# Performance work log

Measured on AMD Instinct MI355X. Metric: run time of the kernel, lower is better.

Reference implementation:

```python
import jax, jax.numpy as jnp
import numpy as np

D_MODEL = 512
D_VALUE = 512
N_HEADS = 8
NEG_INF = -1e30


def _layernorm(x, g, b, eps=1e-5):
    mu = jnp.mean(x, axis=-1, keepdims=True)
    var = jnp.var(x, axis=-1, keepdims=True)
    return (x - mu) * jax.lax.rsqrt(var + eps) * g + b


def setup_inputs() -> dict:
    key = jax.random.key(0)
    ks = jax.random.split(key, 16)
    B, L, dq = 4, 2048, 512
    d_model, d_value, H = D_MODEL, D_VALUE, N_HEADS
    d4 = 4 * d_model
    s = lambda d: 1.0 / np.sqrt(d)
    inp = {
        "q": jax.random.normal(ks[0], (B, L, dq), jnp.float32),
        "k": jax.random.normal(ks[1], (B, L, dq), jnp.float32),
        "v": jax.random.normal(ks[2], (B, L, d_value), jnp.float32),
        "Wq": jax.random.normal(ks[3], (d_model, dq), jnp.float32) * s(dq),
        "bq": jnp.zeros((d_model,), jnp.float32),
        "Wk": jax.random.normal(ks[4], (d_model, dq), jnp.float32) * s(dq),
        "bk": jnp.zeros((d_model,), jnp.float32),
        "Wv": jax.random.normal(ks[5], (d_model, d_value), jnp.float32) * s(d_value),
        "bv": jnp.zeros((d_model,), jnp.float32),
        "Wo": jax.random.normal(ks[6], (d_value, d_model), jnp.float32) * s(d_model),
        "bo": jnp.zeros((d_value,), jnp.float32),
        "Wc1": jax.random.normal(ks[7], (d4, d_value), jnp.float32) * s(d_value),
        "bc1": jnp.zeros((d4,), jnp.float32),
        "Wc2": jax.random.normal(ks[8], (d_value, d4), jnp.float32) * s(d4),
        "bc2": jnp.zeros((d_value,), jnp.float32),
        "g1": jnp.ones((d_value,), jnp.float32),
        "b1": jnp.zeros((d_value,), jnp.float32),
        "g2": jnp.ones((d_value,), jnp.float32),
        "b2": jnp.zeros((d_value,), jnp.float32),
        "Wl": jax.random.normal(ks[9], (d_model, d_value), jnp.float32) * s(d_value),
        "bl": jnp.zeros((d_model,), jnp.float32),
    }
    return inp


def reference(q, k, v, Wq, bq, Wk, bk, Wv, bv, Wo, bo, Wc1, bc1, Wc2, bc2,
              g1, b1, g2, b2, Wl, bl):
    B, L, _ = q.shape
    S = k.shape[1]
    H = N_HEADS
    E = D_MODEL // H
    # projections -> [B, L, H, E]
    queries = (q @ Wq.T + bq).reshape(B, L, H, E)
    keys = (k @ Wk.T + bk).reshape(B, S, H, E)
    values = (v @ Wv.T + bv).reshape(B, S, H, E)
    # naive causal attention, full [B,H,L,S] scores
    scale = 1.0 / np.sqrt(E)
    scores = jnp.einsum('blhe,bshe->bhls', queries, keys)
    causal = jnp.triu(jnp.ones((L, S), dtype=bool), k=1)  # True above diagonal
    scores = jnp.where(causal, NEG_INF, scores)
    A = jax.nn.softmax(scale * scores, axis=-1)
    att = jnp.einsum('bhls,bshd->blhd', A, values).reshape(B, L, H * E)
    att = att @ Wo.T + bo
    # residual + FFN (conv1d kernel_size=1 == pointwise linear)
    x = _layernorm(v + att, g1, b1)
    y = jax.nn.relu(x @ Wc1.T + bc1)
    y = y @ Wc2.T + bc2
    y = _layernorm(x + y, g2, b2)
    return y @ Wl.T + bl
```

## Files before the change

kernel.cpp:

```cpp
#include <hip/hip_runtime.h>
#include <hip/hip_bf16.h>


typedef __attribute__((ext_vector_type(8))) short sh8;
typedef __attribute__((ext_vector_type(4))) float f32x4;

#define QSCALE 0.18033688011110543f

__device__ __forceinline__ void storeOut(float* p, float v) { *p = v; }
__device__ __forceinline__ void storeOut(__hip_bfloat16* p, float v) { *p = __float2bfloat16(v); }

__device__ __forceinline__ void gl_lds16(const void* g, void* l) {
    __builtin_amdgcn_global_load_lds((const __attribute__((address_space(1))) void*)g,
                                     (__attribute__((address_space(3))) void*)l, 16, 0, 0);
}

__device__ __forceinline__ unsigned pk_bf16(float a, float b) {
    __hip_bfloat162 h = __float22bfloat162_rn(make_float2(a, b));
    return *(unsigned*)&h;
}
__device__ __forceinline__ sh8 pk8(float4 a, float4 b) {
    int4 iv = make_int4(pk_bf16(a.x, a.y), pk_bf16(a.z, a.w),
                        pk_bf16(b.x, b.y), pk_bf16(b.z, b.w));
    return *(sh8*)&iv;
}

struct WArg { const float* w[7]; unsigned short* wd; };
__global__ __launch_bounds__(256) void conv_w(WArg p)
{
    const int i = (blockIdx.x * 256 + threadIdx.x) * 4;
    if (i >= 3407872) return;
    const float* s; int off;
    if      (i < 262144)  { s = p.w[0]; off = i; }
    else if (i < 524288)  { s = p.w[1]; off = i - 262144; }
    else if (i < 786432)  { s = p.w[2]; off = i - 524288; }
    else if (i < 1048576) { s = p.w[3]; off = i - 786432; }
    else if (i < 1310720) { s = p.w[4]; off = i - 1048576; }
    else if (i < 2359296) { s = p.w[5]; off = i - 1310720; }
    else                  { s = p.w[6]; off = i - 2359296; }
    const float4 v = *(const float4*)(s + off);
    *(uint2*)(p.wd + i) = make_uint2(pk_bf16(v.x, v.y), pk_bf16(v.z, v.w));
}

struct QkvArg {
    const float *A0, *A1, *A2;
    const float *b0, *b1, *b2;
    unsigned short *C0, *C1;
    unsigned short *Vt;
};
__global__ __launch_bounds__(256) void gemm_qkv(QkvArg ar, const unsigned short* __restrict__ Wall,
                                                int M, int N, int K)
{
    const int z = blockIdx.z;
    const float* A = z == 0 ? ar.A0 : (z == 1 ? ar.A1 : ar.A2);
    const unsigned short* W = Wall + (size_t)z * 262144;
    const float* bias = z == 0 ? ar.b0 : (z == 1 ? ar.b1 : ar.b2);

    __shared__ float AsF[8192];
    __shared__ unsigned short BsL[8192];
    const int t    = threadIdx.x;
    const int wave = t >> 6, lane = t & 63;
    const int quad = lane >> 4, col = lane & 15;
    const int wm   = wave >> 1, wn = wave & 1;
    const int m0   = blockIdx.y * 128, n0 = blockIdx.x * 128;

    f32x4 acc[4][4];
    #pragma unroll
    for (int mt = 0; mt < 4; mt++)
        #pragma unroll
        for (int nt = 0; nt < 4; nt++)
            acc[mt][nt] = (f32x4){0.f, 0.f, 0.f, 0.f};

    for (int k0 = 0; k0 < K; k0 += 64) {
        #pragma unroll
        for (int seg = 0; seg < 8; seg++) {
            const int r0  = (seg * 4 + wave) * 4;
            const int row = r0 + (lane >> 4);
            const int ck  = (lane & 15) ^ (row & 15);
            gl_lds16(A + (size_t)(m0 + row) * K + k0 + ck * 4, &AsF[r0 * 64]);
        }
        #pragma unroll
        for (int seg = 0; seg < 4; seg++) {
            const int r0  = (seg * 4 + wave) * 8;
            const int row = r0 + (lane >> 3);
            const int ck  = (lane & 7) ^ (row & 7);
            gl_lds16(W + (size_t)(n0 + row) * K + k0 + ck * 8, &BsL[r0 * 64]);
        }
        __syncthreads();
        #pragma unroll
        for (int kc = 0; kc < 2; kc++) {
            sh8 af[4], bf[4];
            #pragma unroll
            for (int mt = 0; mt < 4; mt++) {
                const int mr  = wm * 64 + mt * 16 + col;
                const int q0  = kc * 8 + quad * 2;
                const int m16 = mr & 15;
                float4 f0 = *(const float4*)&AsF[mr * 64 + ((q0 ^ m16) << 2)];
                float4 f1 = *(const float4*)&AsF[mr * 64 + (((q0 + 1) ^ m16) << 2)];
                af[mt] = pk8(f0, f1);
            }
            #pragma unroll
            for (int nt = 0; nt < 4; nt++) {
                const int nr = wn * 64 + nt * 16 + col;
                bf[nt] = *(const sh8*)&BsL[nr * 64 + (((kc * 4 + quad) ^ (nr & 7)) << 3)];
            }
            #pragma unroll
            for (int mt = 0; mt < 4; mt++)
                #pragma unroll
                for (int nt = 0; nt < 4; nt++)
                    acc[mt][nt] = __builtin_amdgcn_mfma_f32_16x16x32_bf16(af[mt], bf[nt], acc[mt][nt], 0, 0, 0);
        }
        __syncthreads();
    }

    if (z < 2) {
        unsigned short* C = z == 0 ? ar.C0 : ar.C1;
        const float scale = z == 0 ? QSCALE : 1.0f;
        #pragma unroll
        for (int nt = 0; nt < 4; nt++) {
            const int cn = n0 + wn * 64 + nt * 16 + col;
            const float bj = bias[cn];
            #pragma unroll
            for (int mt = 0; mt < 4; mt++) {
                const int rm = m0 + wm * 64 + mt * 16 + quad * 4;
                #pragma unroll
                for (int reg = 0; reg < 4; reg++)
                    C[(size_t)(rm + reg) * N + cn] =
                        (unsigned short)__bfloat16_as_ushort(__float2bfloat16((acc[mt][nt][reg] + bj) * scale));
            }
        }
    } else {
        const int b = m0 >> 11;
        #pragma unroll
        for (int nt = 0; nt < 4; nt++) {
            const int cn = n0 + wn * 64 + nt * 16 + col;
            const int h = cn >> 6, e = cn & 63;
            const float bj = bias[cn];
            #pragma unroll
            for (int mt = 0; mt < 4; mt++) {
                const int s0r = (m0 + wm * 64 + mt * 16 + quad * 4) & 2047;
                float cv[4];
                #pragma unroll
                for (int reg = 0; reg < 4; reg++) cv[reg] = acc[mt][nt][reg] + bj;
                *(uint2*)(ar.Vt + ((size_t)(b * 8 + h) * 64 + e) * 2048 + s0r) =
                    make_uint2(pk_bf16(cv[0], cv[1]), pk_bf16(cv[2], cv[3]));
            }
        }
    }
}

template <typename TOUT, bool RELU>
__global__ __launch_bounds__(256) void gemm_mfma(const unsigned short* __restrict__ A,
                                                 const unsigned short* __restrict__ W,
                                                 const float* __restrict__ bias,
                                                 TOUT* __restrict__ C,
                                                 int M, int N, int K)
{
    __shared__ unsigned short AsL[8192];
    __shared__ unsigned short BsL[8192];
    const int t    = threadIdx.x;
    const int wave = t >> 6, lane = t & 63;
    const int quad = lane >> 4, col = lane & 15;
    const int wm   = wave >> 1, wn = wave & 1;
    const int m0   = blockIdx.y * 128, n0 = blockIdx.x * 128;

    f32x4 acc[4][4];
    #pragma unroll
    for (int mt = 0; mt < 4; mt++)
        #pragma unroll
        for (int nt = 0; nt < 4; nt++)
            acc[mt][nt] = (f32x4){0.f, 0.f, 0.f, 0.f};

    for (int k0 = 0; k0 < K; k0 += 64) {
        #pragma unroll
        for (int seg = 0; seg < 4; seg++) {
            const int r0  = (seg * 4 + wave) * 8;
            const int row = r0 + (lane >> 3);
            const int ck  = (lane & 7) ^ (row & 7);
            gl_lds16(A + (size_t)(m0 + row) * K + k0 + ck * 8, &AsL[r0 * 64]);
            gl_lds16(W + (size_t)(n0 + row) * K + k0 + ck * 8, &BsL[r0 * 64]);
        }
        __syncthreads();
        #pragma unroll
        for (int kc = 0; kc < 2; kc++) {
            sh8 af[4], bf[4];
            #pragma unroll
            for (int mt = 0; mt < 4; mt++) {
                const int ar = wm * 64 + mt * 16 + col;
                af[mt] = *(const sh8*)&AsL[ar * 64 + (((kc * 4 + quad) ^ (ar & 7)) << 3)];
            }
            #pragma unroll
            for (int nt = 0; nt < 4; nt++) {
                const int nr = wn * 64 + nt * 16 + col;
                bf[nt] = *(const sh8*)&BsL[nr * 64 + (((kc * 4 + quad) ^ (nr & 7)) << 3)];
            }
            #pragma unroll
            for (int mt = 0; mt < 4; mt++)
                #pragma unroll
                for (int nt = 0; nt < 4; nt++)
                    acc[mt][nt] = __builtin_amdgcn_mfma_f32_16x16x32_bf16(af[mt], bf[nt], acc[mt][nt], 0, 0, 0);
        }
        __syncthreads();
    }
    #pragma unroll
    for (int nt = 0; nt < 4; nt++) {
        const int cn = n0 + wn * 64 + nt * 16 + col;
        const float bj = bias[cn];
        #pragma unroll
        for (int mt = 0; mt < 4; mt++) {
            const int rm = m0 + wm * 64 + mt * 16 + quad * 4;
            #pragma unroll
            for (int reg = 0; reg < 4; reg++) {
                float cv = acc[mt][nt][reg] + bj;
                if (RELU) cv = fmaxf(cv, 0.f);
                storeOut(&C[(size_t)(rm + reg) * N + cn], cv);
            }
        }
    }
}

template <typename TOUT, bool RELU>
__global__ __launch_bounds__(256) void gemm_mfma64(const unsigned short* __restrict__ A,
                                                   const unsigned short* __restrict__ W,
                                                   const float* __restrict__ bias,
                                                   TOUT* __restrict__ C,
                                                   int M, int N, int K)
{
    __shared__ unsigned short AsL[4096];
    __shared__ unsigned short BsL[8192];
    const int t    = threadIdx.x;
    const int wave = t >> 6, lane = t & 63;
    const int quad = lane >> 4, col = lane & 15;
    const int wm   = wave >> 1, wn = wave & 1;
    const int m0   = blockIdx.y * 64, n0 = blockIdx.x * 128;

    f32x4 acc[2][4];
    #pragma unroll
    for (int mt = 0; mt < 2; mt++)
        #pragma unroll
        for (int nt = 0; nt < 4; nt++)
            acc[mt][nt] = (f32x4){0.f, 0.f, 0.f, 0.f};

    for (int k0 = 0; k0 < K; k0 += 64) {
        #pragma unroll
        for (int seg = 0; seg < 2; seg++) {
            const int r0  = (seg * 4 + wave) * 8;
            const int row = r0 + (lane >> 3);
            const int ck  = (lane & 7) ^ (row & 7);
            gl_lds16(A + (size_t)(m0 + row) * K + k0 + ck * 8, &AsL[r0 * 64]);
        }
        #pragma unroll
        for (int seg = 0; seg < 4; seg++) {
            const int r0  = (seg * 4 + wave) * 8;
            const int row = r0 + (lane >> 3);
            const int ck  = (lane & 7) ^ (row & 7);
            gl_lds16(W + (size_t)(n0 + row) * K + k0 + ck * 8, &BsL[r0 * 64]);
        }
        __syncthreads();
        #pragma unroll
        for (int kc = 0; kc < 2; kc++) {
            sh8 af[2], bf[4];
            #pragma unroll
            for (int mt = 0; mt < 2; mt++) {
                const int ar = wm * 32 + mt * 16 + col;
                af[mt] = *(const sh8*)&AsL[ar * 64 + (((kc * 4 + quad) ^ (ar & 7)) << 3)];
            }
            #pragma unroll
            for (int nt = 0; nt < 4; nt++) {
                const int nr = wn * 64 + nt * 16 + col;
                bf[nt] = *(const sh8*)&BsL[nr * 64 + (((kc * 4 + quad) ^ (nr & 7)) << 3)];
            }
            #pragma unroll
            for (int mt = 0; mt < 2; mt++)
                #pragma unroll
                for (int nt = 0; nt < 4; nt++)
                    acc[mt][nt] = __builtin_amdgcn_mfma_f32_16x16x32_bf16(af[mt], bf[nt], acc[mt][nt], 0, 0, 0);
        }
        __syncthreads();
    }
    #pragma unroll
    for (int nt = 0; nt < 4; nt++) {
        const int cn = n0 + wn * 64 + nt * 16 + col;
        const float bj = bias[cn];
        #pragma unroll
        for (int mt = 0; mt < 2; mt++) {
            const int rm = m0 + wm * 32 + mt * 16 + quad * 4;
            #pragma unroll
            for (int reg = 0; reg < 4; reg++) {
                float cv = acc[mt][nt][reg] + bj;
                if (RELU) cv = fmaxf(cv, 0.f);
                storeOut(&C[(size_t)(rm + reg) * N + cn], cv);
            }
        }
    }
}

__global__ __launch_bounds__(256, 2) void attn_mfma(const unsigned short* __restrict__ Qb,
                                                    const unsigned short* __restrict__ Kb,
                                                    const unsigned short* __restrict__ Vt,
                                                    __hip_bfloat16* __restrict__ O,
                                                    int L)
{
    __shared__ unsigned short Ks[2][4096];
    __shared__ unsigned short Vs[2][4096];
    __shared__ unsigned short PsA[4][16][72];
    __shared__ unsigned short PsB[4][16][72];

    const int i    = blockIdx.x;
    const int bh   = blockIdx.y;
    const int b    = bh >> 3, h = bh & 7;
    const int t    = threadIdx.x;
    const int w    = t >> 6, lane = t & 63;
    const int quad = lane >> 4, col = lane & 15;

    const int qtA = i, qtB = 31 - i;
    const int qrowA = qtA * 64 + w * 16 + col;
    const int qrowB = qtB * 64 + w * 16 + col;
    const int S = 32 - i;

    const int srow = lane >> 3;
    const int scp  = lane & 7;

    sh8 qfA[2], qfB[2];
    {
        const size_t qa = ((size_t)(b * L + qrowA) * 8 + h) * 64;
        qfA[0] = *(const sh8*)(Qb + qa + quad * 8);
        qfA[1] = *(const sh8*)(Qb + qa + 32 + quad * 8);
        const size_t qb2 = ((size_t)(b * L + qrowB) * 8 + h) * 64;
        qfB[0] = *(const sh8*)(Qb + qb2 + quad * 8);
        qfB[1] = *(const sh8*)(Qb + qb2 + 32 + quad * 8);
    }

    f32x4 OA[4], OB[4];
    #pragma unroll
    for (int nt = 0; nt < 4; nt++) { OA[nt] = (f32x4){0.f,0.f,0.f,0.f}; OB[nt] = (f32x4){0.f,0.f,0.f,0.f}; }
    float lA = 0.f, lB = 0.f;

    {
        #pragma unroll
        for (int seg = 0; seg < 2; seg++) {
            const int r0  = (seg * 4 + w) * 8;
            const int row = r0 + srow;
            const int ck  = scp ^ (row & 7);
            gl_lds16(Kb + ((size_t)(b * L + row) * 8 + h) * 64 + ck * 8, &Ks[0][r0 * 64]);
            gl_lds16(Vt + (size_t)(bh * 64 + row) * L + ck * 8, &Vs[0][r0 * 64]);
        }
        __syncthreads();
    }

    int cur = 0;
    for (int r = 0; r < S; r++) {
        if (r + 1 < S) {
            const int k1 = (r + 1) * 64;
            #pragma unroll
            for (int seg = 0; seg < 2; seg++) {
                const int r0  = (seg * 4 + w) * 8;
                const int row = r0 + srow;
                const int ck  = scp ^ (row & 7);
                gl_lds16(Kb + ((size_t)(b * L + k1 + row) * 8 + h) * 64 + ck * 8, &Ks[cur ^ 1][r0 * 64]);
                gl_lds16(Vt + (size_t)(bh * 64 + row) * L + k1 + ck * 8, &Vs[cur ^ 1][r0 * 64]);
            }
        }

        const int k0 = r * 64;
        const bool actA  = (r <= i);
        const bool maskA = (r == i);
        const bool maskB = (r == S - 1);

        f32x4 stA[4], stB[4];
        const f32x4 zz = {0.f, 0.f, 0.f, 0.f};
        #pragma unroll
        for (int ntk = 0; ntk < 4; ntk++) {
            const int key = ntk * 16 + col;
            const int sw  = key & 7;
            sh8 kf0 = *(const sh8*)&Ks[cur][key * 64 + ((quad ^ sw) << 3)];
            sh8 kf1 = *(const sh8*)&Ks[cur][key * 64 + (((quad + 4) ^ sw) << 3)];
            f32x4 aB = __builtin_amdgcn_mfma_f32_16x16x32_bf16(kf0, qfB[0], zz, 0, 0, 0);
            stB[ntk] = __builtin_amdgcn_mfma_f32_16x16x32_bf16(kf1, qfB[1], aB, 0, 0, 0);
            if (actA) {
                f32x4 aA = __builtin_amdgcn_mfma_f32_16x16x32_bf16(kf0, qfA[0], zz, 0, 0, 0);
                stA[ntk] = __builtin_amdgcn_mfma_f32_16x16x32_bf16(kf1, qfA[1], aA, 0, 0, 0);
            }
        }

        {
            if (maskB) {
                #pragma unroll
                for (int ntk = 0; ntk < 4; ntk++)
                    #pragma unroll
                    for (int reg = 0; reg < 4; reg++)
                        if (k0 + ntk * 16 + quad * 4 + reg > qrowB) stB[ntk][reg] = -1e30f;
            }
            #pragma unroll
            for (int ntk = 0; ntk < 4; ntk++) {
                #pragma unroll
                for (int reg = 0; reg < 4; reg++)
                    stB[ntk][reg] = exp2f(stB[ntk][reg]);
                lB += (stB[ntk][0] + stB[ntk][1]) + (stB[ntk][2] + stB[ntk][3]);
                *(uint2*)&PsB[w][col][ntk * 16 + quad * 4] =
                    make_uint2(pk_bf16(stB[ntk][0], stB[ntk][1]), pk_bf16(stB[ntk][2], stB[ntk][3]));
            }
        }
        if (actA) {
            if (maskA) {
                #pragma unroll
                for (int ntk = 0; ntk < 4; ntk++)
                    #pragma unroll
                    for (int reg = 0; reg < 4; reg++)
                        if (k0 + ntk * 16 + quad * 4 + reg > qrowA) stA[ntk][reg] = -1e30f;
            }
            #pragma unroll
            for (int ntk = 0; ntk < 4; ntk++) {
                #pragma unroll
                for (int reg = 0; reg < 4; reg++)
                    stA[ntk][reg] = exp2f(stA[ntk][reg]);
                lA += (stA[ntk][0] + stA[ntk][1]) + (stA[ntk][2] + stA[ntk][3]);
                *(uint2*)&PsA[w][col][ntk * 16 + quad * 4] =
                    make_uint2(pk_bf16(stA[ntk][0], stA[ntk][1]), pk_bf16(stA[ntk][2], stA[ntk][3]));
            }
        }

        #pragma unroll
        for (int kchunk = 0; kchunk < 2; kchunk++) {
            sh8 pfB = *(const sh8*)&PsB[w][col][kchunk * 32 + quad * 8];
            sh8 pfA;
            if (actA) pfA = *(const sh8*)&PsA[w][col][kchunk * 32 + quad * 8];
            #pragma unroll
            for (int nt = 0; nt < 4; nt++) {
                const int e  = nt * 16 + col;
                sh8 vf = *(const sh8*)&Vs[cur][e * 64 + (((kchunk * 4 + quad) ^ (e & 7)) << 3)];
                OB[nt] = __builtin_amdgcn_mfma_f32_16x16x32_bf16(pfB, vf, OB[nt], 0, 0, 0);
                if (actA) OA[nt] = __builtin_amdgcn_mfma_f32_16x16x32_bf16(pfA, vf, OA[nt], 0, 0, 0);
            }
        }
        __syncthreads();
        cur ^= 1;
    }

    lA += __shfl_xor(lA, 16); lA += __shfl_xor(lA, 32);
    lB += __shfl_xor(lB, 16); lB += __shfl_xor(lB, 32);
    {
        const float li = 1.f / lA;
        float lr[4];
        #pragma unroll
        for (int reg = 0; reg < 4; reg++) lr[reg] = __shfl(li, quad * 4 + reg);
        #pragma unroll
        for (int reg = 0; reg < 4; reg++) {
            const int qr = qtA * 64 + w * 16 + quad * 4 + reg;
            #pragma unroll
            for (int nt = 0; nt < 4; nt++)
                O[((size_t)(b * L + qr) * 8 + h) * 64 + nt * 16 + col] =
                    __float2bfloat16(OA[nt][reg] * lr[reg]);
        }
    }
    {
        const float li = 1.f / lB;
        float lr[4];
        #pragma unroll
        for (int reg = 0; reg < 4; reg++) lr[reg] = __shfl(li, quad * 4 + reg);
        #pragma unroll
        for (int reg = 0; reg < 4; reg++) {
            const int qr = qtB * 64 + w * 16 + quad * 4 + reg;
            #pragma unroll
            for (int nt = 0; nt < 4; nt++)
                O[((size_t)(b * L + qr) * 8 + h) * 64 + nt * 16 + col] =
                    __float2bfloat16(OB[nt][reg] * lr[reg]);
        }
    }
}

__global__ __launch_bounds__(256) void layernorm_k(const float* __restrict__ f1,
                                                   const float* __restrict__ f2,
                                                   const float* __restrict__ rb,
                                                   const float* __restrict__ g,
                                                   const float* __restrict__ bb,
                                                   float* __restrict__ out32,
                                                   __hip_bfloat16* __restrict__ out16)
{
    const int row = blockIdx.x;
    const int t   = threadIdx.x;
    const size_t base = (size_t)row * 512;
    const int i0 = t * 2;

    float a0 = f1[base + i0], a1 = f1[base + i0 + 1];
    if (f2) { a0 += f2[base + i0]; a1 += f2[base + i0 + 1]; }
    if (rb) { a0 += rb[base + i0]; a1 += rb[base + i0 + 1]; }

    float s = a0 + a1, ss = a0 * a0 + a1 * a1;
    #pragma unroll
    for (int off = 32; off > 0; off >>= 1) {
        s  += __shfl_xor(s, off);
        ss += __shfl_xor(ss, off);
    }
    __shared__ float red[16];
    const int lane = t & 63, wid = t >> 6;
    if (lane == 0) { red[wid] = s; red[8 + wid] = ss; }
    __syncthreads();
    if (t == 0) {
        const float S  = red[0] + red[1] + red[2] + red[3];
        const float SS = red[8] + red[9] + red[10] + red[11];
        const float mu = S * (1.f / 512.f);
        const float var = SS * (1.f / 512.f) - mu * mu;
        red[0] = mu;
        red[1] = rsqrtf(fmaxf(var, 0.f) + 1e-5f);
    }
    __syncthreads();
    const float mu = red[0], rstd = red[1];
    const float y0 = (a0 - mu) * rstd * g[i0]     + bb[i0];
    const float y1 = (a1 - mu) * rstd * g[i0 + 1] + bb[i0 + 1];
    if (out32) { out32[base + i0] = y0; out32[base + i0 + 1] = y1; }
    if (out16) { out16[base + i0] = __float2bfloat16(y0); out16[base + i0 + 1] = __float2bfloat16(y1); }
}

extern "C" void kernel_launch(void* const* d_in, const int* in_sizes, int n_in,
                              void* d_out, int out_size, void* d_ws, size_t ws_size,
                              hipStream_t stream)
{
    const float* q   = (const float*)d_in[0];
    const float* k   = (const float*)d_in[1];
    const float* v   = (const float*)d_in[2];
    const float* Wq  = (const float*)d_in[3];
    const float* bq  = (const float*)d_in[4];
    const float* Wk  = (const float*)d_in[5];
    const float* bk  = (const float*)d_in[6];
    const float* Wv  = (const float*)d_in[7];
    const float* bv  = (const float*)d_in[8];
    const float* Wo  = (const float*)d_in[9];
    const float* bo  = (const float*)d_in[10];
    const float* Wc1 = (const float*)d_in[11];
    const float* bc1 = (const float*)d_in[12];
    const float* Wc2 = (const float*)d_in[13];
    const float* bc2 = (const float*)d_in[14];
    const float* g1  = (const float*)d_in[15];
    const float* b1  = (const float*)d_in[16];
    const float* g2  = (const float*)d_in[17];
    const float* b2  = (const float*)d_in[18];
    const float* Wl  = (const float*)d_in[19];
    const float* bl  = (const float*)d_in[20];
    float* out = (float*)d_out;

    const int B = 4, L = 2048, H = 8;
    const int M = B * L;

    char* base = (char*)d_ws;
    unsigned short* Wall = (unsigned short*)(base + 0);
    unsigned short* Wob  = (unsigned short*)(base + 1572864);
    unsigned short* Wlb  = (unsigned short*)(base + 2097152);
    unsigned short* Wc1b = (unsigned short*)(base + 2621440);
    unsigned short* Wc2b = (unsigned short*)(base + 4718592);
    unsigned short* Qb   = (unsigned short*)(base + 6815744);
    unsigned short* Kb   = (unsigned short*)(base + 15204352);
    unsigned short* Vt   = (unsigned short*)(base + 23592960);
    unsigned short* A1   = (unsigned short*)(base + 31981568);
    float*          A2   = (float*)(base + 40370176);
    float*          X1   = (float*)(base + 57147392);
    unsigned short* X1b  = (unsigned short*)(base + 73924608);
    unsigned short* X2b  = (unsigned short*)(base + 73924608);
    unsigned short* H1   = (unsigned short*)(base + 6815744);
    float*          Y2   = (float*)(base + 40370176);

    const dim3 blk(256);

    WArg wa;
    wa.w[0] = Wq; wa.w[1] = Wk; wa.w[2] = Wv; wa.w[3] = Wo; wa.w[4] = Wl;
    wa.w[5] = Wc1; wa.w[6] = Wc2; wa.wd = Wall;
    conv_w<<<dim3(3328), blk, 0, stream>>>(wa);

    QkvArg qa;
    qa.A0 = q;  qa.A1 = k;  qa.A2 = v;
    qa.b0 = bq; qa.b1 = bk; qa.b2 = bv;
    qa.C0 = Qb; qa.C1 = Kb; qa.Vt = Vt;
    gemm_qkv<<<dim3(4, 64, 3), blk, 0, stream>>>(qa, Wall, M, 512, 512);

    attn_mfma<<<dim3(16, B * H), blk, 0, stream>>>(Qb, Kb, Vt, (__hip_bfloat16*)A1, L);

    gemm_mfma64<float, false><<<dim3(4, 128), blk, 0, stream>>>(A1, Wob, bo, A2, M, 512, 512);

    layernorm_k<<<dim3(M), blk, 0, stream>>>(A2, nullptr, v, g1, b1, X1, (__hip_bfloat16*)X1b);

    gemm_mfma<__hip_bfloat16, true><<<dim3(16, 64), blk, 0, stream>>>(X1b, Wc1b, bc1, (__hip_bfloat16*)H1, M, 2048, 512);

    gemm_mfma64<float, false><<<dim3(4, 128), blk, 0, stream>>>(H1, Wc2b, bc2, Y2, M, 512, 2048);

    layernorm_k<<<dim3(M), blk, 0, stream>>>(X1, Y2, nullptr, g2, b2, nullptr, (__hip_bfloat16*)X2b);

    gemm_mfma64<float, false><<<dim3(4, 128), blk, 0, stream>>>(X2b, Wlb, bl, out, M, 512, 512);
}
```

Measured before the change: 323.5 us.

## Load K/V fragments directly from global into registers, drop LDS staging

The attention kernel no longer stages K and V tiles in double-buffered LDS with async global-to-LDS loads and per-iteration barriers. Each wave now loads its own K and V MFMA fragments straight from global memory into registers and prefetches the next tile right after use. This removes the LDS traffic and __syncthreads. In exchange, all four waves redundantly fetch the same K/V data from global/L2, the reads are no longer swizzled or coalesced, and register pressure rises. It also hardcodes the strides 512 and 2048 in place of L.

```diff
diff --git a/kernel.cpp b/kernel.cpp
--- a/kernel.cpp
+++ b/kernel.cpp
@@ -301,8 +301,6 @@
                                                     __hip_bfloat16* __restrict__ O,
                                                     int L)
 {
-    __shared__ unsigned short Ks[2][4096];
-    __shared__ unsigned short Vs[2][4096];
     __shared__ unsigned short PsA[4][16][72];
     __shared__ unsigned short PsB[4][16][72];
 
@@ -317,9 +315,6 @@
     const int qrowA = qtA * 64 + w * 16 + col;
     const int qrowB = qtB * 64 + w * 16 + col;
     const int S = 32 - i;
-
-    const int srow = lane >> 3;
-    const int scp  = lane & 7;
 
     sh8 qfA[2], qfB[2];
     {
@@ -331,37 +326,29 @@
         qfB[1] = *(const sh8*)(Qb + qb2 + 32 + quad * 8);
     }
 
+    const unsigned short* kbase = Kb + ((size_t)(b * L + col)) * 512 + h * 64 + quad * 8;
+    const unsigned short* vbase = Vt + ((size_t)(bh * 64 + col)) * 2048 + quad * 8;
+
+    sh8 kf[8];
+    sh8 vf[8];
+
+    #pragma unroll
+    for (int ntk = 0; ntk < 4; ntk++) {
+        kf[ntk * 2]     = *(const sh8*)(kbase + (size_t)(ntk * 16) * 512);
+        kf[ntk * 2 + 1] = *(const sh8*)(kbase + (size_t)(ntk * 16) * 512 + 32);
+    }
+    #pragma unroll
+    for (int kc = 0; kc < 2; kc++)
+        #pragma unroll
+        for (int nt = 0; nt < 4; nt++)
+            vf[kc * 4 + nt] = *(const sh8*)(vbase + (size_t)(nt * 16) * 2048 + kc * 32);
+
     f32x4 OA[4], OB[4];
     #pragma unroll
     for (int nt = 0; nt < 4; nt++) { OA[nt] = (f32x4){0.f,0.f,0.f,0.f}; OB[nt] = (f32x4){0.f,0.f,0.f,0.f}; }
     float lA = 0.f, lB = 0.f;
 
-    {
-        #pragma unroll
-        for (int seg = 0; seg < 2; seg++) {
-            const int r0  = (seg * 4 + w) * 8;
-            const int row = r0 + srow;
-            const int ck  = scp ^ (row & 7);
-            gl_lds16(Kb + ((size_t)(b * L + row) * 8 + h) * 64 + ck * 8, &Ks[0][r0 * 64]);
-            gl_lds16(Vt + (size_t)(bh * 64 + row) * L + ck * 8, &Vs[0][r0 * 64]);
-        }
-        __syncthreads();
-    }
-
-    int cur = 0;
     for (int r = 0; r < S; r++) {
-        if (r + 1 < S) {
-            const int k1 = (r + 1) * 64;
-            #pragma unroll
-            for (int seg = 0; seg < 2; seg++) {
-                const int r0  = (seg * 4 + w) * 8;
-                const int row = r0 + srow;
-                const int ck  = scp ^ (row & 7);
-                gl_lds16(Kb + ((size_t)(b * L + k1 + row) * 8 + h) * 64 + ck * 8, &Ks[cur ^ 1][r0 * 64]);
-                gl_lds16(Vt + (size_t)(bh * 64 + row) * L + k1 + ck * 8, &Vs[cur ^ 1][r0 * 64]);
-            }
-        }
-
         const int k0 = r * 64;
         const bool actA  = (r <= i);
         const bool maskA = (r == i);
@@ -371,15 +358,20 @@
         const f32x4 zz = {0.f, 0.f, 0.f, 0.f};
         #pragma unroll
         for (int ntk = 0; ntk < 4; ntk++) {
-            const int key = ntk * 16 + col;
-            const int sw  = key & 7;
-            sh8 kf0 = *(const sh8*)&Ks[cur][key * 64 + ((quad ^ sw) << 3)];
-            sh8 kf1 = *(const sh8*)&Ks[cur][key * 64 + (((quad + 4) ^ sw) << 3)];
-            f32x4 aB = __builtin_amdgcn_mfma_f32_16x16x32_bf16(kf0, qfB[0], zz, 0, 0, 0);
-            stB[ntk] = __builtin_amdgcn_mfma_f32_16x16x32_bf16(kf1, qfB[1], aB, 0, 0, 0);
+            f32x4 aB = __builtin_amdgcn_mfma_f32_16x16x32_bf16(kf[ntk * 2], qfB[0], zz, 0, 0, 0);
+            stB[ntk] = __builtin_amdgcn_mfma_f32_16x16x32_bf16(kf[ntk * 2 + 1], qfB[1], aB, 0, 0, 0);
             if (actA) {
-                f32x4 aA = __builtin_amdgcn_mfma_f32_16x16x32_bf16(kf0, qfA[0], zz, 0, 0, 0);
-                stA[ntk] = __builtin_amdgcn_mfma_f32_16x16x32_bf16(kf1, qfA[1], aA, 0, 0, 0);
+                f32x4 aA = __builtin_amdgcn_mfma_f32_16x16x32_bf16(kf[ntk * 2], qfA[0], zz, 0, 0, 0);
+                stA[ntk] = __builtin_amdgcn_mfma_f32_16x16x32_bf16(kf[ntk * 2 + 1], qfA[1], aA, 0, 0, 0);
+            }
+        }
+
+        if (r + 1 < S) {
+            const unsigned short* kb2 = kbase + (size_t)(r + 1) * 64 * 512;
+            #pragma unroll
+            for (int ntk = 0; ntk < 4; ntk++) {
+                kf[ntk * 2]     = *(const sh8*)(kb2 + (size_t)(ntk * 16) * 512);
+                kf[ntk * 2 + 1] = *(const sh8*)(kb2 + (size_t)(ntk * 16) * 512 + 32);
             }
         }
 
@@ -427,14 +419,19 @@
             if (actA) pfA = *(const sh8*)&PsA[w][col][kchunk * 32 + quad * 8];
             #pragma unroll
             for (int nt = 0; nt < 4; nt++) {
-                const int e  = nt * 16 + col;
-                sh8 vf = *(const sh8*)&Vs[cur][e * 64 + (((kchunk * 4 + quad) ^ (e & 7)) << 3)];
-                OB[nt] = __builtin_amdgcn_mfma_f32_16x16x32_bf16(pfB, vf, OB[nt], 0, 0, 0);
-                if (actA) OA[nt] = __builtin_amdgcn_mfma_f32_16x16x32_bf16(pfA, vf, OA[nt], 0, 0, 0);
-            }
-        }
-        __syncthreads();
-        cur ^= 1;
+                OB[nt] = __builtin_amdgcn_mfma_f32_16x16x32_bf16(pfB, vf[kchunk * 4 + nt], OB[nt], 0, 0, 0);
+                if (actA) OA[nt] = __builtin_amdgcn_mfma_f32_16x16x32_bf16(pfA, vf[kchunk * 4 + nt], OA[nt], 0, 0, 0);
+            }
+        }
+
+        if (r + 1 < S) {
+            const unsigned short* vb2 = vbase + (r + 1) * 64;
+            #pragma unroll
+            for (int kc = 0; kc < 2; kc++)
+                #pragma unroll
+                for (int nt = 0; nt < 4; nt++)
+                    vf[kc * 4 + nt] = *(const sh8*)(vb2 + (size_t)(nt * 16) * 2048 + kc * 32);
+        }
     }
 
     lA += __shfl_xor(lA, 16); lA += __shfl_xor(lA, 32);
```

After: 386.4 us. +19.5%, slower.

## Split attention KV range across two blocks and add combine kernel

Applied to the files above, without the earlier changes.

Each attention block's key range is split into two halves handled by separate blocks (split-K), doubling grid size from 512 to 1024 blocks so more CUs are busy. Partial unnormalized outputs and row sums are written in fp32 to workspace, and a new combine kernel sums them, normalizes, and writes bf16. The change also drops K/V double-buffering in favor of a single buffer with a sync per tile, and shares one P scratch buffer between the two query tiles. It adds extra fp32 global traffic and a kernel launch, and may expose load latency now that prefetch is gone.

```diff
diff --git a/kernel.cpp b/kernel.cpp
--- a/kernel.cpp
+++ b/kernel.cpp
@@ -298,15 +298,17 @@
 __global__ __launch_bounds__(256, 2) void attn_mfma(const unsigned short* __restrict__ Qb,
                                                     const unsigned short* __restrict__ Kb,
                                                     const unsigned short* __restrict__ Vt,
-                                                    __hip_bfloat16* __restrict__ O,
+                                                    float* __restrict__ Op,
+                                                    float* __restrict__ Lp,
                                                     int L)
 {
-    __shared__ unsigned short Ks[2][4096];
-    __shared__ unsigned short Vs[2][4096];
-    __shared__ unsigned short PsA[4][16][72];
-    __shared__ unsigned short PsB[4][16][72];
-
-    const int i    = blockIdx.x;
+    __shared__ unsigned short Ks[4096];
+    __shared__ unsigned short Vs[4096];
+    __shared__ unsigned short Ps[4][16][72];
+
+    const int x    = blockIdx.x;
+    const int i    = x >> 1;
+    const int sp   = x & 1;
     const int bh   = blockIdx.y;
     const int b    = bh >> 3, h = bh & 7;
     const int t    = threadIdx.x;
@@ -316,7 +318,10 @@
     const int qtA = i, qtB = 31 - i;
     const int qrowA = qtA * 64 + w * 16 + col;
     const int qrowB = qtB * 64 + w * 16 + col;
-    const int S = 32 - i;
+    const int S  = 32 - i;
+    const int h0 = (S + 1) >> 1;
+    const int r0 = sp ? h0 : 0;
+    const int r1 = sp ? S : h0;
 
     const int srow = lane >> 3;
     const int scp  = lane & 7;
@@ -336,33 +341,18 @@
     for (int nt = 0; nt < 4; nt++) { OA[nt] = (f32x4){0.f,0.f,0.f,0.f}; OB[nt] = (f32x4){0.f,0.f,0.f,0.f}; }
     float lA = 0.f, lB = 0.f;
 
-    {
+    for (int r = r0; r < r1; r++) {
+        const int k0 = r * 64;
         #pragma unroll
         for (int seg = 0; seg < 2; seg++) {
-            const int r0  = (seg * 4 + w) * 8;
-            const int row = r0 + srow;
+            const int rr  = (seg * 4 + w) * 8;
+            const int row = rr + srow;
             const int ck  = scp ^ (row & 7);
-            gl_lds16(Kb + ((size_t)(b * L + row) * 8 + h) * 64 + ck * 8, &Ks[0][r0 * 64]);
-            gl_lds16(Vt + (size_t)(bh * 64 + row) * L + ck * 8, &Vs[0][r0 * 64]);
-        }
-        __syncthreads();
-    }
-
-    int cur = 0;
-    for (int r = 0; r < S; r++) {
-        if (r + 1 < S) {
-            const int k1 = (r + 1) * 64;
-            #pragma unroll
-            for (int seg = 0; seg < 2; seg++) {
-                const int r0  = (seg * 4 + w) * 8;
-                const int row = r0 + srow;
-                const int ck  = scp ^ (row & 7);
-                gl_lds16(Kb + ((size_t)(b * L + k1 + row) * 8 + h) * 64 + ck * 8, &Ks[cur ^ 1][r0 * 64]);
-                gl_lds16(Vt + (size_t)(bh * 64 + row) * L + k1 + ck * 8, &Vs[cur ^ 1][r0 * 64]);
-            }
-        }
-
-        const int k0 = r * 64;
+            gl_lds16(Kb + ((size_t)(b * L + k0 + row) * 8 + h) * 64 + ck * 8, &Ks[rr * 64]);
+            gl_lds16(Vt + (size_t)(bh * 64 + row) * L + k0 + ck * 8, &Vs[rr * 64]);
+        }
+        __syncthreads();
+
         const bool actA  = (r <= i);
         const bool maskA = (r == i);
         const bool maskB = (r == S - 1);
@@ -373,8 +363,8 @@
         for (int ntk = 0; ntk < 4; ntk++) {
             const int key = ntk * 16 + col;
             const int sw  = key & 7;
-            sh8 kf0 = *(const sh8*)&Ks[cur][key * 64 + ((quad ^ sw) << 3)];
-            sh8 kf1 = *(const sh8*)&Ks[cur][key * 64 + (((quad + 4) ^ sw) << 3)];
+            sh8 kf0 = *(const sh8*)&Ks[key * 64 + ((quad ^ sw) << 3)];
+            sh8 kf1 = *(const sh8*)&Ks[key * 64 + (((quad + 4) ^ sw) << 3)];
             f32x4 aB = __builtin_amdgcn_mfma_f32_16x16x32_bf16(kf0, qfB[0], zz, 0, 0, 0);
             stB[ntk] = __builtin_amdgcn_mfma_f32_16x16x32_bf16(kf1, qfB[1], aB, 0, 0, 0);
             if (actA) {
@@ -397,10 +387,21 @@
                 for (int reg = 0; reg < 4; reg++)
                     stB[ntk][reg] = exp2f(stB[ntk][reg]);
                 lB += (stB[ntk][0] + stB[ntk][1]) + (stB[ntk][2] + stB[ntk][3]);
-                *(uint2*)&PsB[w][col][ntk * 16 + quad * 4] =
+                *(uint2*)&Ps[w][col][ntk * 16 + quad * 4] =
                     make_uint2(pk_bf16(stB[ntk][0], stB[ntk][1]), pk_bf16(stB[ntk][2], stB[ntk][3]));
             }
-        }
+            #pragma unroll
+            for (int kchunk = 0; kchunk < 2; kchunk++) {
+                sh8 pf = *(const sh8*)&Ps[w][col][kchunk * 32 + quad * 8];
+                #pragma unroll
+                for (int nt = 0; nt < 4; nt++) {
+                    const int e = nt * 16 + col;
+                    sh8 vf = *(const sh8*)&Vs[e * 64 + (((kchunk * 4 + quad) ^ (e & 7)) << 3)];
+                    OB[nt] = __builtin_amdgcn_mfma_f32_16x16x32_bf16(pf, vf, OB[nt], 0, 0, 0);
+                }
+            }
+        }
+
         if (actA) {
             if (maskA) {
                 #pragma unroll
@@ -415,58 +416,60 @@
                 for (int reg = 0; reg < 4; reg++)
                     stA[ntk][reg] = exp2f(stA[ntk][reg]);
                 lA += (stA[ntk][0] + stA[ntk][1]) + (stA[ntk][2] + stA[ntk][3]);
-                *(uint2*)&PsA[w][col][ntk * 16 + quad * 4] =
+                *(uint2*)&Ps[w][col][ntk * 16 + quad * 4] =
                     make_uint2(pk_bf16(stA[ntk][0], stA[ntk][1]), pk_bf16(stA[ntk][2], stA[ntk][3]));
             }
-        }
-
-        #pragma unroll
-        for (int kchunk = 0; kchunk < 2; kchunk++) {
-            sh8 pfB = *(const sh8*)&PsB[w][col][kchunk * 32 + quad * 8];
-            sh8 pfA;
-            if (actA) pfA = *(const sh8*)&PsA[w][col][kchunk * 32 + quad * 8];
-            #pragma unroll
-            for (int nt = 0; nt < 4; nt++) {
-                const int e  = nt * 16 + col;
-                sh8 vf = *(const sh8*)&Vs[cur][e * 64 + (((kchunk * 4 + quad) ^ (e & 7)) << 3)];
-                OB[nt] = __builtin_amdgcn_mfma_f32_16x16x32_bf16(pfB, vf, OB[nt], 0, 0, 0);
-                if (actA) OA[nt] = __builtin_amdgcn_mfma_f32_16x16x32_bf16(pfA, vf, OA[nt], 0, 0, 0);
-            }
-        }
-        __syncthreads();
-        cur ^= 1;
+            #pragma unroll
+            for (int kchunk = 0; kchunk < 2; kchunk++) {
+                sh8 pf = *(const sh8*)&Ps[w][col][kchunk * 32 + quad * 8];
+                #pragma unroll
+                for (int nt = 0; nt < 4; nt++) {
+                    const int e = nt * 16 + col;
+                    sh8 vf = *(const sh8*)&Vs[e * 64 + (((kchunk * 4 + quad) ^ (e & 7)) << 3)];
+                    OA[nt] = __builtin_amdgcn_mfma_f32_16x16x32_bf16(pf, vf, OA[nt], 0, 0, 0);
+                }
+            }
+        }
+        __syncthreads();
     }
 
     lA += __shfl_xor(lA, 16); lA += __shfl_xor(lA, 32);
     lB += __shfl_xor(lB, 16); lB += __shfl_xor(lB, 32);
     {
-        const float li = 1.f / lA;
-        float lr[4];
-        #pragma unroll
-        for (int reg = 0; reg < 4; reg++) lr[reg] = __shfl(li, quad * 4 + reg);
+        float* Od = Op + (size_t)sp * 4194304;
+        float* Ld = Lp + (size_t)sp * 65536;
+        if (quad == 0) {
+            Ld[(size_t)(b * L + qtA * 64 + w * 16 + col) * 8 + h] = lA;
+            Ld[(size_t)(b * L + qtB * 64 + w * 16 + col) * 8 + h] = lB;
+        }
         #pragma unroll
         for (int reg = 0; reg < 4; reg++) {
-            const int qr = qtA * 64 + w * 16 + quad * 4 + reg;
-            #pragma unroll
-            for (int nt = 0; nt < 4; nt++)
-                O[((size_t)(b * L + qr) * 8 + h) * 64 + nt * 16 + col] =
-                    __float2bfloat16(OA[nt][reg] * lr[reg]);
-        }
-    }
-    {
-        const float li = 1.f / lB;
-        float lr[4];
-        #pragma unroll
-        for (int reg = 0; reg < 4; reg++) lr[reg] = __shfl(li, quad * 4 + reg);
-        #pragma unroll
-        for (int reg = 0; reg < 4; reg++) {
-            const int qr = qtB * 64 + w * 16 + quad * 4 + reg;
-            #pragma unroll
-            for (int nt = 0; nt < 4; nt++)
-                O[((size_t)(b * L + qr) * 8 + h) * 64 + nt * 16 + col] =
-                    __float2bfloat16(OB[nt][reg] * lr[reg]);
-        }
-    }
+            const int qrA = qtA * 64 + w * 16 + quad * 4 + reg;
+            const int qrB = qtB * 64 + w * 16 + quad * 4 + reg;
+            #pragma unroll
+            for (int nt = 0; nt < 4; nt++) {
+                Od[((size_t)(b * L + qrA) * 8 + h) * 64 + nt * 16 + col] = OA[nt][reg];
+                Od[((size_t)(b * L + qrB) * 8 + h) * 64 + nt * 16 + col] = OB[nt][reg];
+            }
+        }
+    }
+}
+
+__global__ __launch_bounds__(256) void attn_combine(const float* __restrict__ Op,
+                                                    const float* __restrict__ Lp,
+                                                    unsigned short* __restrict__ O)
+{
+    const int row = blockIdx.x;
+    const int t   = threadIdx.x;
+    const int e   = t * 2;
+    const int h   = e >> 6;
+    const float l0 = Lp[(size_t)row * 8 + h];
+    const float l1 = Lp[65536 + (size_t)row * 8 + h];
+    const float inv = 1.f / (l0 + l1);
+    const size_t idx = (size_t)row * 512 + e;
+    const float2 o0 = *(const float2*)(Op + idx);
+    const float2 o1 = *(const float2*)(Op + 4194304 + idx);
+    *(unsigned*)&O[idx] = pk_bf16((o0.x + o1.x) * inv, (o0.y + o1.y) * inv);
 }
 
 __global__ __launch_bounds__(256) void layernorm_k(const float* __restrict__ f1,
@@ -552,6 +555,8 @@
     unsigned short* Kb   = (unsigned short*)(base + 15204352);
     unsigned short* Vt   = (unsigned short*)(base + 23592960);
     unsigned short* A1   = (unsigned short*)(base + 31981568);
+    float*          Oprt = (float*)(base + 40370176);
+    float*          Lprt = (float*)(base + 73924608);
     float*          A2   = (float*)(base + 40370176);
     float*          X1   = (float*)(base + 57147392);
     unsigned short* X1b  = (unsigned short*)(base + 73924608);
@@ -572,7 +577,9 @@
     qa.C0 = Qb; qa.C1 = Kb; qa.Vt = Vt;
     gemm_qkv<<<dim3(4, 64, 3), blk, 0, stream>>>(qa, Wall, M, 512, 512);
 
-    attn_mfma<<<dim3(16, B * H), blk, 0, stream>>>(Qb, Kb, Vt, (__hip_bfloat16*)A1, L);
+    attn_mfma<<<dim3(32, B * H), blk, 0, stream>>>(Qb, Kb, Vt, Oprt, Lprt, L);
+
+    attn_combine<<<dim3(M), blk, 0, stream>>>(Oprt, Lprt, A1);
 
     gemm_mfma64<float, false><<<dim3(4, 128), blk, 0, stream>>>(A1, Wob, bo, A2, M, 512, 512);
 
```

Result: slower. 330.8 us (+2.3%).

## Double-buffer GEMM LDS staging and pre-convert QKV inputs to bf16

Applied to the files above, without the earlier changes.

Adds a kernel that converts q, k, v to bf16 once so the QKV projection GEMM loads bf16 tiles directly instead of loading fp32 into LDS and packing per fragment. All GEMM kernels now use two LDS buffers, issuing the next k-tile's global-to-LDS loads before computing on the current one, with a launch-bounds occupancy hint. The cost is an extra conversion pass over the inputs and doubled LDS per block, which may reduce occupancy.

```diff
diff --git a/kernel.cpp b/kernel.cpp
--- a/kernel.cpp
+++ b/kernel.cpp
@@ -18,11 +18,6 @@
 __device__ __forceinline__ unsigned pk_bf16(float a, float b) {
     __hip_bfloat162 h = __float22bfloat162_rn(make_float2(a, b));
     return *(unsigned*)&h;
-}
-__device__ __forceinline__ sh8 pk8(float4 a, float4 b) {
-    int4 iv = make_int4(pk_bf16(a.x, a.y), pk_bf16(a.z, a.w),
-                        pk_bf16(b.x, b.y), pk_bf16(b.z, b.w));
-    return *(sh8*)&iv;
 }
 
 struct WArg { const float* w[7]; unsigned short* wd; };
@@ -42,67 +37,78 @@
     *(uint2*)(p.wd + i) = make_uint2(pk_bf16(v.x, v.y), pk_bf16(v.z, v.w));
 }
 
+__global__ __launch_bounds__(256) void conv_in(const float* __restrict__ q,
+                                               const float* __restrict__ k,
+                                               const float* __restrict__ v,
+                                               unsigned short* __restrict__ dst)
+{
+    const int i = (blockIdx.x * 256 + threadIdx.x) * 4;
+    if (i >= 12582912) return;
+    const float* s; int off;
+    if      (i < 4194304) { s = q; off = i; }
+    else if (i < 8388608) { s = k; off = i - 4194304; }
+    else                  { s = v; off = i - 8388608; }
+    const float4 x = *(const float4*)(s + off);
+    *(uint2*)(dst + i) = make_uint2(pk_bf16(x.x, x.y), pk_bf16(x.z, x.w));
+}
+
 struct QkvArg {
-    const float *A0, *A1, *A2;
+    const unsigned short *A0, *A1, *A2;
     const float *b0, *b1, *b2;
     unsigned short *C0, *C1;
     unsigned short *Vt;
 };
-__global__ __launch_bounds__(256) void gemm_qkv(QkvArg ar, const unsigned short* __restrict__ Wall,
-                                                int M, int N, int K)
+__global__ __launch_bounds__(256, 2) void gemm_qkv(QkvArg ar, const unsigned short* __restrict__ Wall,
+                                                   int M, int N, int K)
 {
     const int z = blockIdx.z;
-    const float* A = z == 0 ? ar.A0 : (z == 1 ? ar.A1 : ar.A2);
+    const unsigned short* A = z == 0 ? ar.A0 : (z == 1 ? ar.A1 : ar.A2);
     const unsigned short* W = Wall + (size_t)z * 262144;
     const float* bias = z == 0 ? ar.b0 : (z == 1 ? ar.b1 : ar.b2);
 
-    __shared__ float AsF[8192];
-    __shared__ unsigned short BsL[8192];
+    __shared__ unsigned short AsL[2][8192];
+    __shared__ unsigned short BsL[2][8192];
     const int t    = threadIdx.x;
     const int wave = t >> 6, lane = t & 63;
     const int quad = lane >> 4, col = lane & 15;
     const int wm   = wave >> 1, wn = wave & 1;
     const int m0   = blockIdx.y * 128, n0 = blockIdx.x * 128;
 
-    f32x4 acc[4][4];
-    #pragma unroll
-    for (int mt = 0; mt < 4; mt++)
-        #pragma unroll
-        for (int nt = 0; nt < 4; nt++)
-            acc[mt][nt] = (f32x4){0.f, 0.f, 0.f, 0.f};
-
-    for (int k0 = 0; k0 < K; k0 += 64) {
-        #pragma unroll
-        for (int seg = 0; seg < 8; seg++) {
-            const int r0  = (seg * 4 + wave) * 4;
-            const int row = r0 + (lane >> 4);
-            const int ck  = (lane & 15) ^ (row & 15);
-            gl_lds16(A + (size_t)(m0 + row) * K + k0 + ck * 4, &AsF[r0 * 64]);
-        }
+    auto stage = [&](int k0, int buf) {
         #pragma unroll
         for (int seg = 0; seg < 4; seg++) {
             const int r0  = (seg * 4 + wave) * 8;
             const int row = r0 + (lane >> 3);
             const int ck  = (lane & 7) ^ (row & 7);
-            gl_lds16(W + (size_t)(n0 + row) * K + k0 + ck * 8, &BsL[r0 * 64]);
-        }
-        __syncthreads();
+            gl_lds16(A + (size_t)(m0 + row) * K + k0 + ck * 8, &AsL[buf][r0 * 64]);
+            gl_lds16(W + (size_t)(n0 + row) * K + k0 + ck * 8, &BsL[buf][r0 * 64]);
+        }
+    };
+
+    f32x4 acc[4][4];
+    #pragma unroll
+    for (int mt = 0; mt < 4; mt++)
+        #pragma unroll
+        for (int nt = 0; nt < 4; nt++)
+            acc[mt][nt] = (f32x4){0.f, 0.f, 0.f, 0.f};
+
+    stage(0, 0);
+    __syncthreads();
+    int cur = 0;
+    for (int k0 = 0; k0 < K; k0 += 64) {
+        if (k0 + 64 < K) stage(k0 + 64, cur ^ 1);
         #pragma unroll
         for (int kc = 0; kc < 2; kc++) {
             sh8 af[4], bf[4];
             #pragma unroll
             for (int mt = 0; mt < 4; mt++) {
-                const int mr  = wm * 64 + mt * 16 + col;
-                const int q0  = kc * 8 + quad * 2;
-                const int m16 = mr & 15;
-                float4 f0 = *(const float4*)&AsF[mr * 64 + ((q0 ^ m16) << 2)];
-                float4 f1 = *(const float4*)&AsF[mr * 64 + (((q0 + 1) ^ m16) << 2)];
-                af[mt] = pk8(f0, f1);
+                const int arow = wm * 64 + mt * 16 + col;
+                af[mt] = *(const sh8*)&AsL[cur][arow * 64 + (((kc * 4 + quad) ^ (arow & 7)) << 3)];
             }
             #pragma unroll
             for (int nt = 0; nt < 4; nt++) {
                 const int nr = wn * 64 + nt * 16 + col;
-                bf[nt] = *(const sh8*)&BsL[nr * 64 + (((kc * 4 + quad) ^ (nr & 7)) << 3)];
+                bf[nt] = *(const sh8*)&BsL[cur][nr * 64 + (((kc * 4 + quad) ^ (nr & 7)) << 3)];
             }
             #pragma unroll
             for (int mt = 0; mt < 4; mt++)
@@ -111,6 +117,7 @@
                     acc[mt][nt] = __builtin_amdgcn_mfma_f32_16x16x32_bf16(af[mt], bf[nt], acc[mt][nt], 0, 0, 0);
         }
         __syncthreads();
+        cur ^= 1;
     }
 
     if (z < 2) {
@@ -150,49 +157,55 @@
 }
 
 template <typename TOUT, bool RELU>
-__global__ __launch_bounds__(256) void gemm_mfma(const unsigned short* __restrict__ A,
-                                                 const unsigned short* __restrict__ W,
-                                                 const float* __restrict__ bias,
-                                                 TOUT* __restrict__ C,
-                                                 int M, int N, int K)
-{
-    __shared__ unsigned short AsL[8192];
-    __shared__ unsigned short BsL[8192];
+__global__ __launch_bounds__(256, 2) void gemm_mfma(const unsigned short* __restrict__ A,
+                                                    const unsigned short* __restrict__ W,
+                                                    const float* __restrict__ bias,
+                                                    TOUT* __restrict__ C,
+                                                    int M, int N, int K)
+{
+    __shared__ unsigned short AsL[2][8192];
+    __shared__ unsigned short BsL[2][8192];
     const int t    = threadIdx.x;
     const int wave = t >> 6, lane = t & 63;
     const int quad = lane >> 4, col = lane & 15;
     const int wm   = wave >> 1, wn = wave & 1;
     const int m0   = blockIdx.y * 128, n0 = blockIdx.x * 128;
 
-    f32x4 acc[4][4];
-    #pragma unroll
-    for (int mt = 0; mt < 4; mt++)
-        #pragma unroll
-        for (int nt = 0; nt < 4; nt++)
-            acc[mt][nt] = (f32x4){0.f, 0.f, 0.f, 0.f};
-
-    for (int k0 = 0; k0 < K; k0 += 64) {
+    auto stage = [&](int k0, int buf) {
         #pragma unroll
         for (int seg = 0; seg < 4; seg++) {
             const int r0  = (seg * 4 + wave) * 8;
             const int row = r0 + (lane >> 3);
             const int ck  = (lane & 7) ^ (row & 7);
-            gl_lds16(A + (size_t)(m0 + row) * K + k0 + ck * 8, &AsL[r0 * 64]);
-            gl_lds16(W + (size_t)(n0 + row) * K + k0 + ck * 8, &BsL[r0 * 64]);
-        }
-        __syncthreads();
+            gl_lds16(A + (size_t)(m0 + row) * K + k0 + ck * 8, &AsL[buf][r0 * 64]);
+            gl_lds16(W + (size_t)(n0 + row) * K + k0 + ck * 8, &BsL[buf][r0 * 64]);
+        }
+    };
+
+    f32x4 acc[4][4];
+    #pragma unroll
+    for (int mt = 0; mt < 4; mt++)
+        #pragma unroll
+        for (int nt = 0; nt < 4; nt++)
+            acc[mt][nt] = (f32x4){0.f, 0.f, 0.f, 0.f};
+
+    stage(0, 0);
+    __syncthreads();
+    int cur = 0;
+    for (int k0 = 0; k0 < K; k0 += 64) {
+        if (k0 + 64 < K) stage(k0 + 64, cur ^ 1);
         #pragma unroll
         for (int kc = 0; kc < 2; kc++) {
             sh8 af[4], bf[4];
             #pragma unroll
             for (int mt = 0; mt < 4; mt++) {
                 const int ar = wm * 64 + mt * 16 + col;
-                af[mt] = *(const sh8*)&AsL[ar * 64 + (((kc * 4 + quad) ^ (ar & 7)) << 3)];
+                af[mt] = *(const sh8*)&AsL[cur][ar * 64 + (((kc * 4 + quad) ^ (ar & 7)) << 3)];
             }
             #pragma unroll
             for (int nt = 0; nt < 4; nt++) {
                 const int nr = wn * 64 + nt * 16 + col;
-                bf[nt] = *(const sh8*)&BsL[nr * 64 + (((kc * 4 + quad) ^ (nr & 7)) << 3)];
+                bf[nt] = *(const sh8*)&BsL[cur][nr * 64 + (((kc * 4 + quad) ^ (nr & 7)) << 3)];
             }
             #pragma unroll
             for (int mt = 0; mt < 4; mt++)
@@ -201,6 +214,7 @@
                     acc[mt][nt] = __builtin_amdgcn_mfma_f32_16x16x32_bf16(af[mt], bf[nt], acc[mt][nt], 0, 0, 0);
         }
         __syncthreads();
+        cur ^= 1;
     }
     #pragma unroll
     for (int nt = 0; nt < 4; nt++) {
@@ -220,55 +234,61 @@
 }
 
 template <typename TOUT, bool RELU>
-__global__ __launch_bounds__(256) void gemm_mfma64(const unsigned short* __restrict__ A,
-                                                   const unsigned short* __restrict__ W,
-                                                   const float* __restrict__ bias,
-                                                   TOUT* __restrict__ C,
-                                                   int M, int N, int K)
-{
-    __shared__ unsigned short AsL[4096];
-    __shared__ unsigned short BsL[8192];
+__global__ __launch_bounds__(256, 2) void gemm_mfma64(const unsigned short* __restrict__ A,
+                                                      const unsigned short* __restrict__ W,
+                                                      const float* __restrict__ bias,
+                                                      TOUT* __restrict__ C,
+                                                      int M, int N, int K)
+{
+    __shared__ unsigned short AsL[2][4096];
+    __shared__ unsigned short BsL[2][8192];
     const int t    = threadIdx.x;
     const int wave = t >> 6, lane = t & 63;
     const int quad = lane >> 4, col = lane & 15;
     const int wm   = wave >> 1, wn = wave & 1;
     const int m0   = blockIdx.y * 64, n0 = blockIdx.x * 128;
 
-    f32x4 acc[2][4];
-    #pragma unroll
-    for (int mt = 0; mt < 2; mt++)
-        #pragma unroll
-        for (int nt = 0; nt < 4; nt++)
-            acc[mt][nt] = (f32x4){0.f, 0.f, 0.f, 0.f};
-
-    for (int k0 = 0; k0 < K; k0 += 64) {
+    auto stage = [&](int k0, int buf) {
         #pragma unroll
         for (int seg = 0; seg < 2; seg++) {
             const int r0  = (seg * 4 + wave) * 8;
             const int row = r0 + (lane >> 3);
             const int ck  = (lane & 7) ^ (row & 7);
-            gl_lds16(A + (size_t)(m0 + row) * K + k0 + ck * 8, &AsL[r0 * 64]);
+            gl_lds16(A + (size_t)(m0 + row) * K + k0 + ck * 8, &AsL[buf][r0 * 64]);
         }
         #pragma unroll
         for (int seg = 0; seg < 4; seg++) {
             const int r0  = (seg * 4 + wave) * 8;
             const int row = r0 + (lane >> 3);
             const int ck  = (lane & 7) ^ (row & 7);
-            gl_lds16(W + (size_t)(n0 + row) * K + k0 + ck * 8, &BsL[r0 * 64]);
-        }
-        __syncthreads();
+            gl_lds16(W + (size_t)(n0 + row) * K + k0 + ck * 8, &BsL[buf][r0 * 64]);
+        }
+    };
+
+    f32x4 acc[2][4];
+    #pragma unroll
+    for (int mt = 0; mt < 2; mt++)
+        #pragma unroll
+        for (int nt = 0; nt < 4; nt++)
+            acc[mt][nt] = (f32x4){0.f, 0.f, 0.f, 0.f};
+
+    stage(0, 0);
+    __syncthreads();
+    int cur = 0;
+    for (int k0 = 0; k0 < K; k0 += 64) {
+        if (k0 + 64 < K) stage(k0 + 64, cur ^ 1);
         #pragma unroll
         for (int kc = 0; kc < 2; kc++) {
             sh8 af[2], bf[4];
             #pragma unroll
             for (int mt = 0; mt < 2; mt++) {
                 const int ar = wm * 32 + mt * 16 + col;
-                af[mt] = *(const sh8*)&AsL[ar * 64 + (((kc * 4 + quad) ^ (ar & 7)) << 3)];
+                af[mt] = *(const sh8*)&AsL[cur][ar * 64 + (((kc * 4 + quad) ^ (ar & 7)) << 3)];
             }
             #pragma unroll
             for (int nt = 0; nt < 4; nt++) {
                 const int nr = wn * 64 + nt * 16 + col;
-                bf[nt] = *(const sh8*)&BsL[nr * 64 + (((kc * 4 + quad) ^ (nr & 7)) << 3)];
+                bf[nt] = *(const sh8*)&BsL[cur][nr * 64 + (((kc * 4 + quad) ^ (nr & 7)) << 3)];
             }
             #pragma unroll
             for (int mt = 0; mt < 2; mt++)
@@ -277,6 +297,7 @@
                     acc[mt][nt] = __builtin_amdgcn_mfma_f32_16x16x32_bf16(af[mt], bf[nt], acc[mt][nt], 0, 0, 0);
         }
         __syncthreads();
+        cur ^= 1;
     }
     #pragma unroll
     for (int nt = 0; nt < 4; nt++) {
@@ -552,6 +573,7 @@
     unsigned short* Kb   = (unsigned short*)(base + 15204352);
     unsigned short* Vt   = (unsigned short*)(base + 23592960);
     unsigned short* A1   = (unsigned short*)(base + 31981568);
+    unsigned short* Ab   = (unsigned short*)(base + 40370176);
     float*          A2   = (float*)(base + 40370176);
     float*          X1   = (float*)(base + 57147392);
     unsigned short* X1b  = (unsigned short*)(base + 73924608);
@@ -566,8 +588,10 @@
     wa.w[5] = Wc1; wa.w[6] = Wc2; wa.wd = Wall;
     conv_w<<<dim3(3328), blk, 0, stream>>>(wa);
 
+    conv_in<<<dim3(12288), blk, 0, stream>>>(q, k, v, Ab);
+
     QkvArg qa;
-    qa.A0 = q;  qa.A1 = k;  qa.A2 = v;
+    qa.A0 = Ab; qa.A1 = Ab + 4194304; qa.A2 = Ab + 8388608;
     qa.b0 = bq; qa.b1 = bk; qa.b2 = bv;
     qa.C0 = Qb; qa.C1 = Kb; qa.Vt = Vt;
     gemm_qkv<<<dim3(4, 64, 3), blk, 0, stream>>>(qa, Wall, M, 512, 512);
```

After: 318.8 us. No clear change (-1.4%).
